# Kernel tuning notes

Hardware: AMD Instinct MI355X
Metric: run time of the kernel (lower is better)

The kernel has to match this reference:

```python
import jax, jax.numpy as jnp
import numpy as np

B, Q, KV, D, H = 2, 2048, 2048, 1024, 16
HD = D // H  # head dim = 64


def setup_inputs() -> dict:
    key = jax.random.key(0)
    ks = jax.random.split(key, 16)
    s = 1.0 / np.sqrt(D)
    return {
        "q": jax.random.normal(ks[0], (B, Q, D), jnp.float32),
        "k": jax.random.normal(ks[1], (B, KV, D), jnp.float32),
        "v": jax.random.normal(ks[2], (B, KV, D), jnp.float32),
        "past_k": jax.random.normal(ks[3], (B, KV, D), jnp.float32),
        "past_v": jax.random.normal(ks[4], (B, KV, D), jnp.float32),
        "mask": jax.random.randint(ks[5], (B, Q, KV + KV), 0, 2).astype(bool),
        "Wq": jax.random.uniform(ks[6], (D, D), jnp.float32, -s, s),
        "bq": jax.random.uniform(ks[7], (D,), jnp.float32, -s, s),
        "Wk": jax.random.uniform(ks[8], (D, D), jnp.float32, -s, s),
        "bk": jax.random.uniform(ks[9], (D,), jnp.float32, -s, s),
        "Wv": jax.random.uniform(ks[10], (D, D), jnp.float32, -s, s),
        "bv": jax.random.uniform(ks[11], (D,), jnp.float32, -s, s),
        "Wl": jax.random.uniform(ks[12], (D, D), jnp.float32, -s, s),
        "bl": jax.random.uniform(ks[13], (D,), jnp.float32, -s, s),
    }


def _split_heads(x):
    # (B, S, D) -> (B, H, S, HD)
    b, s, _ = x.shape
    return x.reshape(b, s, H, HD).transpose(0, 2, 1, 3)


def reference(q, k, v, past_k, past_v, mask, Wq, bq, Wk, bk, Wv, bv, Wl, bl):
    qp = q @ Wq.T + bq
    kp = k @ Wk.T + bk
    vp = v @ Wv.T + bv
    k_cat = jnp.concatenate([past_k, kp], axis=-2)  # (B, P+KV, D)
    v_cat = jnp.concatenate([past_v, vp], axis=-2)
    qh = _split_heads(qp)        # (B, H, Q, HD)
    kh = _split_heads(k_cat)     # (B, H, P+KV, HD)
    vh = _split_heads(v_cat)
    scores = jnp.einsum("bhqd,bhkd->bhqk", qh, kh) / np.sqrt(HD)
    scores = scores + mask[:, None].astype(scores.dtype) * (-10000.0)
    attn = jax.nn.softmax(scores, axis=-1)
    out = jnp.einsum("bhqk,bhkd->bhqd", attn, vh)  # (B, H, Q, HD)
    out = out.transpose(0, 2, 1, 3).reshape(q.shape[0], q.shape[1], D)
    x = out @ Wl.T + bl
    return (x, k_cat, v_cat)
```

## Files before the change

kernel.cpp:

```cpp
#include <hip/hip_runtime.h>

#define QLEN 2048
#define KVTOT 4096
#define DMODEL 1024
#define MASKC -10000.0f
#define SENT  -20000.0f

typedef __attribute__((ext_vector_type(8))) short bf16x8;
typedef __attribute__((ext_vector_type(4))) float f32x4;
typedef unsigned short u16;
typedef unsigned int u32;
typedef unsigned long long u64;

__device__ __forceinline__ u16 f2b(float f) {
  union { float f; unsigned u; } v; v.f = f;
  unsigned r = v.u + 0x7FFFu + ((v.u >> 16) & 1u);
  return (u16)(r >> 16);
}

__device__ __forceinline__ u32 cvt_pk_bf16(float lo, float hi) {
  u32 r;
  asm("v_cvt_pk_bf16_f32 %0, %1, %2" : "=v"(r) : "v"(lo), "v"(hi));
  return r;
}

__device__ __forceinline__ void gll16(const u16* g, u16* l) {
  __builtin_amdgcn_global_load_lds(
      (const __attribute__((address_space(1))) u32*)g,
      (__attribute__((address_space(3))) u32*)l, 16, 0, 0);
}

__global__ __launch_bounds__(256) void copy_past(
    const float* __restrict__ pk, const float* __restrict__ pv,
    float* __restrict__ kcat, float* __restrict__ vcat,
    u16* __restrict__ kh) {
  int i = blockIdx.x * 256 + threadIdx.x;
  int b = i >> 19;
  int r = i & 524287;
  size_t src = (size_t)i * 4;
  size_t dst = ((size_t)b * 1048576 + r) * 4;
  float4 kk = *(const float4*)&pk[src];
  float4 vv = *(const float4*)&pv[src];
  *(float4*)&kcat[dst] = kk;
  *(float4*)&vcat[dst] = vv;
  int s = r >> 8;
  int c4 = (r & 255) * 4;
  int h = c4 >> 6, d = c4 & 63;
  uint2 w = make_uint2(cvt_pk_bf16(kk.x, kk.y), cvt_pk_bf16(kk.z, kk.w));
  *(uint2*)&kh[((size_t)(b * 16 + h) * KVTOT + s) * 64 + d] = w;
}

__global__ __launch_bounds__(256) void maskpack(
    const int* __restrict__ mask, u64* __restrict__ bits) {
  int w = blockIdx.x * 4 + (threadIdx.x >> 6);
  int lane = threadIdx.x & 63;
  int mv = mask[(size_t)w * 64 + lane];
  u64 b = __ballot(mv != 0);
  if (lane == 0) bits[w] = b;
}

__global__ __launch_bounds__(256) void w2b(
    const float* __restrict__ w0, const float* __restrict__ w1,
    const float* __restrict__ w2, const float* __restrict__ w3,
    u16* __restrict__ dst) {
  const float* src = blockIdx.y == 0 ? w0 : blockIdx.y == 1 ? w1
                   : blockIdx.y == 2 ? w2 : w3;
  size_t i = ((size_t)blockIdx.x * 256 + threadIdx.x) * 8;
  float4 a = *(const float4*)&src[i];
  float4 b = *(const float4*)&src[i + 4];
  uint4 o = {cvt_pk_bf16(a.x, a.y), cvt_pk_bf16(a.z, a.w),
             cvt_pk_bf16(b.x, b.y), cvt_pk_bf16(b.z, b.w)};
  *(uint4*)&dst[(size_t)blockIdx.y * 1048576 + i] = o;
}

__global__ __launch_bounds__(256) void gemm_qkv(
    const float* __restrict__ qA, const float* __restrict__ kA,
    const float* __restrict__ vA, const u16* __restrict__ Wb,
    const float* __restrict__ bq, const float* __restrict__ bk,
    const float* __restrict__ bv,
    u16* __restrict__ qh, float* __restrict__ kcat, u16* __restrict__ kh,
    float* __restrict__ vcat) {
  const int K = 1024, N = 1024;
  __shared__ u16 As[128][32];
  __shared__ u16 Bs[128][32];
  const int z = blockIdx.z;
  const float* A = (z == 0) ? qA : (z == 1) ? kA : vA;
  const u16* W = Wb + (size_t)z * 1048576;
  const float* bias = (z == 0) ? bq : (z == 1) ? bk : bv;
  const int t = threadIdx.x;
  const int m0 = blockIdx.y * 128, n0 = blockIdx.x * 128;
  const int lane = t & 63, wid = t >> 6;
  const int wr = (wid >> 1) * 64, wc = (wid & 1) * 64;
  const int lr = lane & 15, lg = lane >> 4;
  const int ko = lg * 8;

  f32x4 acc[4][4];
  #pragma unroll
  for (int m = 0; m < 4; ++m)
    #pragma unroll
    for (int n = 0; n < 4; ++n)
      acc[m][n] = (f32x4){0.f, 0.f, 0.f, 0.f};

  for (int k0 = 0; k0 < K; k0 += 32) {
    float4 a0[2], a1[2];
    #pragma unroll
    for (int j = 0; j < 2; ++j) {
      int idx = t + j * 256;
      int r = idx >> 2, c8 = (idx & 3) * 8;
      const float* ap = A + (size_t)(m0 + r) * K + k0 + c8;
      a0[j] = *(const float4*)ap;
      a1[j] = *(const float4*)(ap + 4);
    }
    __syncthreads();
    #pragma unroll
    for (int j = 0; j < 2; ++j) {
      int idx = t + j * 256;
      int r = idx >> 2, c8 = (idx & 3) * 8;
      gll16(W + (size_t)(n0 + r) * K + k0 + c8,
            &Bs[0][0] + (size_t)(j * 256 + (t & ~63)) * 8);
      uint4 o = {cvt_pk_bf16(a0[j].x, a0[j].y), cvt_pk_bf16(a0[j].z, a0[j].w),
                 cvt_pk_bf16(a1[j].x, a1[j].y), cvt_pk_bf16(a1[j].z, a1[j].w)};
      *(uint4*)&As[r][c8] = o;
    }
    __syncthreads();
    bf16x8 av[4], bv4[4];
    #pragma unroll
    for (int m = 0; m < 4; ++m)
      av[m] = *(const bf16x8*)&As[wr + m * 16 + lr][ko];
    #pragma unroll
    for (int n = 0; n < 4; ++n)
      bv4[n] = *(const bf16x8*)&Bs[wc + n * 16 + lr][ko];
    #pragma unroll
    for (int m = 0; m < 4; ++m)
      #pragma unroll
      for (int n = 0; n < 4; ++n)
        acc[m][n] = __builtin_amdgcn_mfma_f32_16x16x32_bf16(av[m], bv4[n], acc[m][n], 0, 0, 0);
  }

  const int rq = lg * 4;
  #pragma unroll
  for (int m = 0; m < 4; ++m) {
    #pragma unroll
    for (int r = 0; r < 4; ++r) {
      int row = m0 + wr + m * 16 + rq + r;
      int bb = row >> 11, s = row & 2047;
      #pragma unroll
      for (int n = 0; n < 4; ++n) {
        int col = n0 + wc + n * 16 + lr;
        float val = acc[m][n][r] + bias[col];
        int hh = col >> 6, d = col & 63;
        if (z == 0) {
          qh[((size_t)(bb * 16 + hh) * QLEN + s) * 64 + d] = f2b(val * 0.125f);
        } else if (z == 1) {
          kcat[(size_t)(bb * 4096 + 2048 + s) * 1024 + col] = val;
          kh[((size_t)(bb * 16 + hh) * KVTOT + 2048 + s) * 64 + d] = f2b(val);
        } else {
          vcat[(size_t)(bb * 4096 + 2048 + s) * 1024 + col] = val;
        }
      }
    }
  }
}

__global__ __launch_bounds__(256) void gemm_out(
    const u16* __restrict__ A, const u16* __restrict__ W,
    const float* __restrict__ bias, float* __restrict__ C) {
  const int K = 1024, N = 1024;
  __shared__ u16 As[128][32];
  __shared__ u16 Bs[128][32];
  const int t = threadIdx.x;
  const int m0 = blockIdx.y * 128, n0 = blockIdx.x * 128;
  const int lane = t & 63, wid = t >> 6;
  const int wr = (wid >> 1) * 64, wc = (wid & 1) * 64;
  const int lr = lane & 15, lg = lane >> 4;
  const int ko = lg * 8;

  f32x4 acc[4][4];
  #pragma unroll
  for (int m = 0; m < 4; ++m)
    #pragma unroll
    for (int n = 0; n < 4; ++n)
      acc[m][n] = (f32x4){0.f, 0.f, 0.f, 0.f};

  for (int k0 = 0; k0 < K; k0 += 32) {
    __syncthreads();
    #pragma unroll
    for (int j = 0; j < 2; ++j) {
      int idx = t + j * 256;
      int r = idx >> 2, c8 = (idx & 3) * 8;
      size_t ldsoff = (size_t)(j * 256 + (t & ~63)) * 8;
      gll16(A + (size_t)(m0 + r) * K + k0 + c8, &As[0][0] + ldsoff);
      gll16(W + (size_t)(n0 + r) * K + k0 + c8, &Bs[0][0] + ldsoff);
    }
    __syncthreads();
    bf16x8 av[4], bv4[4];
    #pragma unroll
    for (int m = 0; m < 4; ++m)
      av[m] = *(const bf16x8*)&As[wr + m * 16 + lr][ko];
    #pragma unroll
    for (int n = 0; n < 4; ++n)
      bv4[n] = *(const bf16x8*)&Bs[wc + n * 16 + lr][ko];
    #pragma unroll
    for (int m = 0; m < 4; ++m)
      #pragma unroll
      for (int n = 0; n < 4; ++n)
        acc[m][n] = __builtin_amdgcn_mfma_f32_16x16x32_bf16(av[m], bv4[n], acc[m][n], 0, 0, 0);
  }

  const int rq = lg * 4;
  #pragma unroll
  for (int m = 0; m < 4; ++m) {
    #pragma unroll
    for (int r = 0; r < 4; ++r) {
      int row = m0 + wr + m * 16 + rq + r;
      float* cp = C + (size_t)row * N;
      #pragma unroll
      for (int n = 0; n < 4; ++n) {
        int col = n0 + wc + n * 16 + lr;
        cp[col] = acc[m][n][r] + bias[col];
      }
    }
  }
}

__global__ __launch_bounds__(256) void repack_vt(
    const float* __restrict__ src, u16* __restrict__ dst) {
  __shared__ u16 T[64][72];
  const int t = threadIdx.x;
  const int kv0 = blockIdx.x * 64;
  const int bh = blockIdx.y;
  const int b = bh >> 4, h = bh & 15;
  #pragma unroll
  for (int it = 0; it < 4; ++it) {
    int idx = t + it * 256;
    int r = idx >> 4;
    int c4 = (idx & 15) * 4;
    float4 v = *(const float4*)(src + (size_t)(b * KVTOT + kv0 + r) * DMODEL + h * 64 + c4);
    *(uint2*)&T[r][c4] = make_uint2(cvt_pk_bf16(v.x, v.y), cvt_pk_bf16(v.z, v.w));
  }
  __syncthreads();
  #pragma unroll
  for (int it = 0; it < 2; ++it) {
    int idx = t + it * 256;
    int d = idx & 63;
    int kc8 = (idx >> 6) * 8;
    bf16x8 o;
    #pragma unroll
    for (int j = 0; j < 8; ++j) o[j] = (short)T[kc8 + j][d];
    *(bf16x8*)(dst + (size_t)((b * 16 + h) * 64 + d) * KVTOT + kv0 + kc8) = o;
  }
}

__global__ __launch_bounds__(256) void attn_mfma(
    const u16* __restrict__ qh, const u16* __restrict__ kh,
    const u16* __restrict__ vt, const u64* __restrict__ mbits,
    u16* __restrict__ out) {
  __shared__ u16 Kl[64][72];
  __shared__ u16 Vl[64][72];
  __shared__ u16 Pl[4][16][72];
  const int t = threadIdx.x;
  const int wid = t >> 6, lane = t & 63;
  const int lr = lane & 15, lg = lane >> 4;
  const int fid = blockIdx.x;
  const int virt = (fid & 7) * 128 + (fid >> 3);
  const int bh = virt >> 5, qt = virt & 31;
  const int b = bh >> 4, h = bh & 15;
  const int qw = qt * 64 + wid * 16;

  bf16x8 ones;
  #pragma unroll
  for (int j = 0; j < 8; ++j) ones[j] = (short)0x3F80;

  bf16x8 qf[2];
  {
    const u16* qp = qh + ((size_t)bh * QLEN + qw + lr) * 64 + lg * 8;
    qf[0] = *(const bf16x8*)qp;
    qf[1] = *(const bf16x8*)(qp + 32);
  }

  const size_t khb = (size_t)bh * KVTOT * 64;
  const size_t vtb = (size_t)bh * 64 * KVTOT;
  const u64* mrow = mbits + ((size_t)b * QLEN + qw + lr) * (KVTOT / 64);

  bf16x8 kreg[2], vreg[2];
  #pragma unroll
  for (int j = 0; j < 2; ++j) {
    int idx = t + j * 256;
    int r = idx >> 3, c8 = (idx & 7) * 8;
    kreg[j] = *(const bf16x8*)(kh + khb + (size_t)r * 64 + c8);
    vreg[j] = *(const bf16x8*)(vt + vtb + (size_t)r * KVTOT + c8);
  }

  float mprev = SENT;
  f32x4 oacc[5];
  #pragma unroll
  for (int dt = 0; dt < 5; ++dt) oacc[dt] = (f32x4){0.f, 0.f, 0.f, 0.f};

  for (int it = 0; it < KVTOT / 64; ++it) {
    u64 mb = mrow[it];
    __syncthreads();
    #pragma unroll
    for (int j = 0; j < 2; ++j) {
      int idx = t + j * 256;
      int r = idx >> 3, c8 = (idx & 7) * 8;
      *(bf16x8*)&Kl[r][c8] = kreg[j];
      *(bf16x8*)&Vl[r][c8] = vreg[j];
    }
    __syncthreads();
    if (it + 1 < KVTOT / 64) {
      int t0n = (it + 1) * 64;
      #pragma unroll
      for (int j = 0; j < 2; ++j) {
        int idx = t + j * 256;
        int r = idx >> 3, c8 = (idx & 7) * 8;
        kreg[j] = *(const bf16x8*)(kh + khb + (size_t)(t0n + r) * 64 + c8);
        vreg[j] = *(const bf16x8*)(vt + vtb + (size_t)r * KVTOT + t0n + c8);
      }
    }

    const u64 mq = mb >> (lg * 4);
    const float negm = -mprev, negmm = MASKC - mprev;
    f32x4 sacc[4];
    __builtin_amdgcn_s_setprio(1);
    #pragma unroll
    for (int tile = 0; tile < 4; ++tile) {
      unsigned nib = (unsigned)((mq >> (tile * 16)) & 0xFull);
      #pragma unroll
      for (int r = 0; r < 4; ++r)
        sacc[tile][r] = (nib & (1u << r)) ? negmm : negm;
      bf16x8 kf0 = *(const bf16x8*)&Kl[tile * 16 + lr][lg * 8];
      bf16x8 kf1 = *(const bf16x8*)&Kl[tile * 16 + lr][32 + lg * 8];
      sacc[tile] = __builtin_amdgcn_mfma_f32_16x16x32_bf16(kf0, qf[0], sacc[tile], 0, 0, 0);
      sacc[tile] = __builtin_amdgcn_mfma_f32_16x16x32_bf16(kf1, qf[1], sacc[tile], 0, 0, 0);
    }
    __builtin_amdgcn_s_setprio(0);

    float rmax = fmaxf(fmaxf(fmaxf(sacc[0][0], sacc[0][1]), fmaxf(sacc[0][2], sacc[0][3])),
                       fmaxf(fmaxf(sacc[1][0], sacc[1][1]), fmaxf(sacc[1][2], sacc[1][3])));
    rmax = fmaxf(rmax, fmaxf(fmaxf(fmaxf(sacc[2][0], sacc[2][1]), fmaxf(sacc[2][2], sacc[2][3])),
                             fmaxf(fmaxf(sacc[3][0], sacc[3][1]), fmaxf(sacc[3][2], sacc[3][3]))));
    rmax = fmaxf(rmax, __shfl_xor(rmax, 16));
    rmax = fmaxf(rmax, __shfl_xor(rmax, 32));

    if (__all(rmax <= 8.0f)) {
      #pragma unroll
      for (int tile = 0; tile < 4; ++tile) {
        float p0 = __expf(sacc[tile][0]);
        float p1 = __expf(sacc[tile][1]);
        float p2 = __expf(sacc[tile][2]);
        float p3 = __expf(sacc[tile][3]);
        *(uint2*)&Pl[wid][lr][tile * 16 + lg * 4] =
            make_uint2(cvt_pk_bf16(p0, p1), cvt_pk_bf16(p2, p3));
      }
    } else {
      float shift = fmaxf(rmax, 0.f);
      float corr = __expf(-shift);
      float cr[4];
      #pragma unroll
      for (int r = 0; r < 4; ++r) cr[r] = __shfl(corr, lg * 4 + r);
      #pragma unroll
      for (int dt = 0; dt < 5; ++dt)
        #pragma unroll
        for (int r = 0; r < 4; ++r) oacc[dt][r] *= cr[r];
      mprev += shift;
      #pragma unroll
      for (int tile = 0; tile < 4; ++tile) {
        float p0 = __expf(sacc[tile][0] - shift);
        float p1 = __expf(sacc[tile][1] - shift);
        float p2 = __expf(sacc[tile][2] - shift);
        float p3 = __expf(sacc[tile][3] - shift);
        *(uint2*)&Pl[wid][lr][tile * 16 + lg * 4] =
            make_uint2(cvt_pk_bf16(p0, p1), cvt_pk_bf16(p2, p3));
      }
    }

    bf16x8 pa0 = *(const bf16x8*)&Pl[wid][lr][lg * 8];
    bf16x8 pa1 = *(const bf16x8*)&Pl[wid][lr][32 + lg * 8];
    __builtin_amdgcn_s_setprio(1);
    #pragma unroll
    for (int dt = 0; dt < 4; ++dt) {
      bf16x8 vb0 = *(const bf16x8*)&Vl[dt * 16 + lr][lg * 8];
      bf16x8 vb1 = *(const bf16x8*)&Vl[dt * 16 + lr][32 + lg * 8];
      oacc[dt] = __builtin_amdgcn_mfma_f32_16x16x32_bf16(pa0, vb0, oacc[dt], 0, 0, 0);
      oacc[dt] = __builtin_amdgcn_mfma_f32_16x16x32_bf16(pa1, vb1, oacc[dt], 0, 0, 0);
    }
    oacc[4] = __builtin_amdgcn_mfma_f32_16x16x32_bf16(pa0, ones, oacc[4], 0, 0, 0);
    oacc[4] = __builtin_amdgcn_mfma_f32_16x16x32_bf16(pa1, ones, oacc[4], 0, 0, 0);
    __builtin_amdgcn_s_setprio(0);
  }

  #pragma unroll
  for (int r = 0; r < 4; ++r) {
    float inv = 1.f / oacc[4][r];
    #pragma unroll
    for (int dt = 0; dt < 4; ++dt)
      out[((size_t)b * QLEN + qw + lg * 4 + r) * DMODEL + h * 64 + dt * 16 + lr] =
          f2b(oacc[dt][r] * inv);
  }
}

extern "C" void kernel_launch(void* const* d_in, const int* in_sizes, int n_in,
                              void* d_out, int out_size, void* d_ws, size_t ws_size,
                              hipStream_t stream) {
  const float* q      = (const float*)d_in[0];
  const float* k      = (const float*)d_in[1];
  const float* v      = (const float*)d_in[2];
  const float* past_k = (const float*)d_in[3];
  const float* past_v = (const float*)d_in[4];
  const int*   mask   = (const int*)d_in[5];
  const float* Wq     = (const float*)d_in[6];
  const float* bq     = (const float*)d_in[7];
  const float* Wk     = (const float*)d_in[8];
  const float* bk     = (const float*)d_in[9];
  const float* Wv     = (const float*)d_in[10];
  const float* bv     = (const float*)d_in[11];
  const float* Wl     = (const float*)d_in[12];
  const float* bl     = (const float*)d_in[13];

  float* xout = (float*)d_out;
  float* kcat = xout + 4194304;
  float* vcat = xout + 12582912;

  u16* wsb = (u16*)d_ws;
  u16* attno = wsb;
  u16* qh = wsb + 4194304;
  u16* kh = wsb + 8388608;
  u16* vt = wsb + 16777216;
  u16* Wb = wsb + 25165824;
  u64* mbits = (u64*)(wsb + 29360128);

  copy_past<<<4096, 256, 0, stream>>>(past_k, past_v, kcat, vcat, kh);
  maskpack<<<65536, 256, 0, stream>>>(mask, mbits);
  w2b<<<dim3(512, 4), 256, 0, stream>>>(Wq, Wk, Wv, Wl, Wb);

  gemm_qkv<<<dim3(8, 32, 3), 256, 0, stream>>>(
      q, k, v, Wb, bq, bk, bv, qh, kcat, kh, vcat);

  repack_vt<<<dim3(64, 32), 256, 0, stream>>>(vcat, vt);

  attn_mfma<<<1024, 256, 0, stream>>>(qh, kh, vt, mbits, attno);

  gemm_out<<<dim3(8, 32), 256, 0, stream>>>(attno, Wb + 3145728, bl, xout);
}
```

Baseline: 323.3 us.

## Split KV across waves with register-resident K/V and merge partial softmax

Result: slower. 332.1 us (+2.7%).

```diff
diff --git a/kernel.cpp b/kernel.cpp
--- a/kernel.cpp
+++ b/kernel.cpp
@@ -3,8 +3,8 @@
 #define QLEN 2048
 #define KVTOT 4096
 #define DMODEL 1024
-#define MASKC -10000.0f
-#define SENT  -20000.0f
+#define MASKC2 -14427.0f
+#define SENT2  -28854.0f
 
 typedef __attribute__((ext_vector_type(8))) short bf16x8;
 typedef __attribute__((ext_vector_type(4))) float f32x4;
@@ -21,6 +21,18 @@
 __device__ __forceinline__ u32 cvt_pk_bf16(float lo, float hi) {
   u32 r;
   asm("v_cvt_pk_bf16_f32 %0, %1, %2" : "=v"(r) : "v"(lo), "v"(hi));
+  return r;
+}
+
+__device__ __forceinline__ float exp2v(float x) {
+  float r;
+  asm("v_exp_f32 %0, %1" : "=v"(r) : "v"(x));
+  return r;
+}
+
+__device__ __forceinline__ float max3f(float a, float b, float c) {
+  float r;
+  asm("v_max3_f32 %0, %1, %2, %3" : "=v"(r) : "v"(a), "v"(b), "v"(c));
   return r;
 }
 
@@ -150,7 +162,7 @@
         float val = acc[m][n][r] + bias[col];
         int hh = col >> 6, d = col & 63;
         if (z == 0) {
-          qh[((size_t)(bb * 16 + hh) * QLEN + s) * 64 + d] = f2b(val * 0.125f);
+          qh[((size_t)(bb * 16 + hh) * QLEN + s) * 64 + d] = f2b(val * 0.18033688f);
         } else if (z == 1) {
           kcat[(size_t)(bb * 4096 + 2048 + s) * 1024 + col] = val;
           kh[((size_t)(bb * 16 + hh) * KVTOT + 2048 + s) * 64 + d] = f2b(val);
@@ -251,12 +263,13 @@
   }
 }
 
-__global__ __launch_bounds__(256) void attn_mfma(
+__global__ __launch_bounds__(256, 2) void attn_mfma(
     const u16* __restrict__ qh, const u16* __restrict__ kh,
     const u16* __restrict__ vt, const u64* __restrict__ mbits,
     u16* __restrict__ out) {
-  __shared__ u16 Kl[64][72];
-  __shared__ u16 Vl[64][72];
+  __shared__ float mO[4][64][68];
+  __shared__ float mM[4][64];
+  __shared__ float mL[4][64];
   __shared__ u16 Pl[4][16][72];
   const int t = threadIdx.x;
   const int wid = t >> 6, lane = t & 63;
@@ -265,138 +278,182 @@
   const int virt = (fid & 7) * 128 + (fid >> 3);
   const int bh = virt >> 5, qt = virt & 31;
   const int b = bh >> 4, h = bh & 15;
-  const int qw = qt * 64 + wid * 16;
+  const int q0 = qt * 64;
 
   bf16x8 ones;
   #pragma unroll
   for (int j = 0; j < 8; ++j) ones[j] = (short)0x3F80;
 
-  bf16x8 qf[2];
-  {
-    const u16* qp = qh + ((size_t)bh * QLEN + qw + lr) * 64 + lg * 8;
-    qf[0] = *(const bf16x8*)qp;
-    qf[1] = *(const bf16x8*)(qp + 32);
-  }
-
-  const size_t khb = (size_t)bh * KVTOT * 64;
-  const size_t vtb = (size_t)bh * 64 * KVTOT;
-  const u64* mrow = mbits + ((size_t)b * QLEN + qw + lr) * (KVTOT / 64);
-
-  bf16x8 kreg[2], vreg[2];
-  #pragma unroll
-  for (int j = 0; j < 2; ++j) {
-    int idx = t + j * 256;
-    int r = idx >> 3, c8 = (idx & 7) * 8;
-    kreg[j] = *(const bf16x8*)(kh + khb + (size_t)r * 64 + c8);
-    vreg[j] = *(const bf16x8*)(vt + vtb + (size_t)r * KVTOT + c8);
-  }
-
-  float mprev = SENT;
-  f32x4 oacc[5];
-  #pragma unroll
-  for (int dt = 0; dt < 5; ++dt) oacc[dt] = (f32x4){0.f, 0.f, 0.f, 0.f};
-
-  for (int it = 0; it < KVTOT / 64; ++it) {
-    u64 mb = mrow[it];
-    __syncthreads();
-    #pragma unroll
-    for (int j = 0; j < 2; ++j) {
-      int idx = t + j * 256;
-      int r = idx >> 3, c8 = (idx & 7) * 8;
-      *(bf16x8*)&Kl[r][c8] = kreg[j];
-      *(bf16x8*)&Vl[r][c8] = vreg[j];
-    }
-    __syncthreads();
-    if (it + 1 < KVTOT / 64) {
-      int t0n = (it + 1) * 64;
-      #pragma unroll
-      for (int j = 0; j < 2; ++j) {
-        int idx = t + j * 256;
-        int r = idx >> 3, c8 = (idx & 7) * 8;
-        kreg[j] = *(const bf16x8*)(kh + khb + (size_t)(t0n + r) * 64 + c8);
-        vreg[j] = *(const bf16x8*)(vt + vtb + (size_t)r * KVTOT + t0n + c8);
-      }
-    }
-
-    const u64 mq = mb >> (lg * 4);
-    const float negm = -mprev, negmm = MASKC - mprev;
-    f32x4 sacc[4];
-    __builtin_amdgcn_s_setprio(1);
-    #pragma unroll
-    for (int tile = 0; tile < 4; ++tile) {
-      unsigned nib = (unsigned)((mq >> (tile * 16)) & 0xFull);
-      #pragma unroll
-      for (int r = 0; r < 4; ++r)
-        sacc[tile][r] = (nib & (1u << r)) ? negmm : negm;
-      bf16x8 kf0 = *(const bf16x8*)&Kl[tile * 16 + lr][lg * 8];
-      bf16x8 kf1 = *(const bf16x8*)&Kl[tile * 16 + lr][32 + lg * 8];
-      sacc[tile] = __builtin_amdgcn_mfma_f32_16x16x32_bf16(kf0, qf[0], sacc[tile], 0, 0, 0);
-      sacc[tile] = __builtin_amdgcn_mfma_f32_16x16x32_bf16(kf1, qf[1], sacc[tile], 0, 0, 0);
-    }
-    __builtin_amdgcn_s_setprio(0);
-
-    float rmax = fmaxf(fmaxf(fmaxf(sacc[0][0], sacc[0][1]), fmaxf(sacc[0][2], sacc[0][3])),
-                       fmaxf(fmaxf(sacc[1][0], sacc[1][1]), fmaxf(sacc[1][2], sacc[1][3])));
-    rmax = fmaxf(rmax, fmaxf(fmaxf(fmaxf(sacc[2][0], sacc[2][1]), fmaxf(sacc[2][2], sacc[2][3])),
-                             fmaxf(fmaxf(sacc[3][0], sacc[3][1]), fmaxf(sacc[3][2], sacc[3][3]))));
-    rmax = fmaxf(rmax, __shfl_xor(rmax, 16));
-    rmax = fmaxf(rmax, __shfl_xor(rmax, 32));
-
-    if (__all(rmax <= 8.0f)) {
+  bf16x8 qf[4][2];
+  #pragma unroll
+  for (int i = 0; i < 4; ++i) {
+    const u16* qp = qh + ((size_t)bh * QLEN + q0 + i * 16 + lr) * 64 + lg * 8;
+    qf[i][0] = *(const bf16x8*)qp;
+    qf[i][1] = *(const bf16x8*)(qp + 32);
+  }
+
+  const u16* kbase = kh + (size_t)bh * KVTOT * 64 + (size_t)wid * 1024 * 64;
+  const u16* vbase = vt + (size_t)bh * 64 * KVTOT + wid * 1024;
+  const u64* mbase = mbits + ((size_t)b * QLEN + q0 + lr) * 64 + wid * 16;
+
+  float mprev[4] = {SENT2, SENT2, SENT2, SENT2};
+  f32x4 oacc[4][4];
+  f32x4 oaccL[4];
+  #pragma unroll
+  for (int i = 0; i < 4; ++i) {
+    oaccL[i] = (f32x4){0.f, 0.f, 0.f, 0.f};
+    #pragma unroll
+    for (int dt = 0; dt < 4; ++dt) oacc[i][dt] = (f32x4){0.f, 0.f, 0.f, 0.f};
+  }
+
+  bf16x8 kf[4][2];
+  #pragma unroll
+  for (int tile = 0; tile < 4; ++tile) {
+    const u16* kp = kbase + (size_t)(tile * 16 + lr) * 64 + lg * 8;
+    kf[tile][0] = *(const bf16x8*)kp;
+    kf[tile][1] = *(const bf16x8*)(kp + 32);
+  }
+
+  for (int it = 0; it < 16; ++it) {
+    bf16x8 vf[4][2];
+    const u16* vp = vbase + it * 64;
+    #pragma unroll
+    for (int dt = 0; dt < 4; ++dt) {
+      const u16* vq = vp + (size_t)(dt * 16 + lr) * KVTOT + lg * 8;
+      vf[dt][0] = *(const bf16x8*)vq;
+      vf[dt][1] = *(const bf16x8*)(vq + 32);
+    }
+
+    #pragma unroll
+    for (int i = 0; i < 4; ++i) {
+      u64 mb = mbase[(size_t)i * 1024 + it];
+      u64 mq = mb >> (lg * 4);
+      const float negm = -mprev[i], negmm = MASKC2 - mprev[i];
+      f32x4 sacc[4];
       #pragma unroll
       for (int tile = 0; tile < 4; ++tile) {
-        float p0 = __expf(sacc[tile][0]);
-        float p1 = __expf(sacc[tile][1]);
-        float p2 = __expf(sacc[tile][2]);
-        float p3 = __expf(sacc[tile][3]);
+        unsigned nib = (unsigned)((mq >> (tile * 16)) & 0xFull);
+        #pragma unroll
+        for (int r = 0; r < 4; ++r)
+          sacc[tile][r] = (nib & (1u << r)) ? negmm : negm;
+      }
+      __builtin_amdgcn_s_setprio(1);
+      #pragma unroll
+      for (int tile = 0; tile < 4; ++tile) {
+        sacc[tile] = __builtin_amdgcn_mfma_f32_16x16x32_bf16(kf[tile][0], qf[i][0], sacc[tile], 0, 0, 0);
+        sacc[tile] = __builtin_amdgcn_mfma_f32_16x16x32_bf16(kf[tile][1], qf[i][1], sacc[tile], 0, 0, 0);
+      }
+      __builtin_amdgcn_s_setprio(0);
+
+      if (i == 3 && it + 1 < 16) {
+        const u16* kp = kbase + (size_t)(it + 1) * 4096;
+        #pragma unroll
+        for (int tile = 0; tile < 4; ++tile) {
+          const u16* kq = kp + (size_t)(tile * 16 + lr) * 64 + lg * 8;
+          kf[tile][0] = *(const bf16x8*)kq;
+          kf[tile][1] = *(const bf16x8*)(kq + 32);
+        }
+      }
+
+      float t1 = max3f(sacc[0][0], sacc[0][1], sacc[0][2]);
+      float t2 = max3f(sacc[0][3], sacc[1][0], sacc[1][1]);
+      float t3 = max3f(sacc[1][2], sacc[1][3], sacc[2][0]);
+      float t4 = max3f(sacc[2][1], sacc[2][2], sacc[2][3]);
+      float t5 = max3f(sacc[3][0], sacc[3][1], sacc[3][2]);
+      float rmax = fmaxf(sacc[3][3], t1);
+      rmax = max3f(rmax, t2, t3);
+      rmax = max3f(rmax, t4, t5);
+      rmax = fmaxf(rmax, __shfl_xor(rmax, 16));
+      rmax = fmaxf(rmax, __shfl_xor(rmax, 32));
+
+      if (!__all(rmax <= 11.0f)) {
+        float shift = fmaxf(rmax, 0.f);
+        float corr = exp2v(-shift);
+        float cr[4];
+        #pragma unroll
+        for (int r = 0; r < 4; ++r) cr[r] = __shfl(corr, lg * 4 + r);
+        #pragma unroll
+        for (int dt = 0; dt < 4; ++dt)
+          #pragma unroll
+          for (int r = 0; r < 4; ++r) oacc[i][dt][r] *= cr[r];
+        #pragma unroll
+        for (int r = 0; r < 4; ++r) oaccL[i][r] *= cr[r];
+        mprev[i] += shift;
+        #pragma unroll
+        for (int tile = 0; tile < 4; ++tile)
+          #pragma unroll
+          for (int r = 0; r < 4; ++r) sacc[tile][r] -= shift;
+      }
+
+      #pragma unroll
+      for (int tile = 0; tile < 4; ++tile) {
+        float p0 = exp2v(sacc[tile][0]);
+        float p1 = exp2v(sacc[tile][1]);
+        float p2 = exp2v(sacc[tile][2]);
+        float p3 = exp2v(sacc[tile][3]);
         *(uint2*)&Pl[wid][lr][tile * 16 + lg * 4] =
             make_uint2(cvt_pk_bf16(p0, p1), cvt_pk_bf16(p2, p3));
       }
-    } else {
-      float shift = fmaxf(rmax, 0.f);
-      float corr = __expf(-shift);
-      float cr[4];
-      #pragma unroll
-      for (int r = 0; r < 4; ++r) cr[r] = __shfl(corr, lg * 4 + r);
-      #pragma unroll
-      for (int dt = 0; dt < 5; ++dt)
-        #pragma unroll
-        for (int r = 0; r < 4; ++r) oacc[dt][r] *= cr[r];
-      mprev += shift;
-      #pragma unroll
-      for (int tile = 0; tile < 4; ++tile) {
-        float p0 = __expf(sacc[tile][0] - shift);
-        float p1 = __expf(sacc[tile][1] - shift);
-        float p2 = __expf(sacc[tile][2] - shift);
-        float p3 = __expf(sacc[tile][3] - shift);
-        *(uint2*)&Pl[wid][lr][tile * 16 + lg * 4] =
-            make_uint2(cvt_pk_bf16(p0, p1), cvt_pk_bf16(p2, p3));
-      }
-    }
-
-    bf16x8 pa0 = *(const bf16x8*)&Pl[wid][lr][lg * 8];
-    bf16x8 pa1 = *(const bf16x8*)&Pl[wid][lr][32 + lg * 8];
-    __builtin_amdgcn_s_setprio(1);
-    #pragma unroll
-    for (int dt = 0; dt < 4; ++dt) {
-      bf16x8 vb0 = *(const bf16x8*)&Vl[dt * 16 + lr][lg * 8];
-      bf16x8 vb1 = *(const bf16x8*)&Vl[dt * 16 + lr][32 + lg * 8];
-      oacc[dt] = __builtin_amdgcn_mfma_f32_16x16x32_bf16(pa0, vb0, oacc[dt], 0, 0, 0);
-      oacc[dt] = __builtin_amdgcn_mfma_f32_16x16x32_bf16(pa1, vb1, oacc[dt], 0, 0, 0);
-    }
-    oacc[4] = __builtin_amdgcn_mfma_f32_16x16x32_bf16(pa0, ones, oacc[4], 0, 0, 0);
-    oacc[4] = __builtin_amdgcn_mfma_f32_16x16x32_bf16(pa1, ones, oacc[4], 0, 0, 0);
-    __builtin_amdgcn_s_setprio(0);
-  }
-
-  #pragma unroll
-  for (int r = 0; r < 4; ++r) {
-    float inv = 1.f / oacc[4][r];
+      bf16x8 pa0 = *(const bf16x8*)&Pl[wid][lr][lg * 8];
+      bf16x8 pa1 = *(const bf16x8*)&Pl[wid][lr][32 + lg * 8];
+
+      __builtin_amdgcn_s_setprio(1);
+      #pragma unroll
+      for (int dt = 0; dt < 4; ++dt) {
+        oacc[i][dt] = __builtin_amdgcn_mfma_f32_16x16x32_bf16(pa0, vf[dt][0], oacc[i][dt], 0, 0, 0);
+        oacc[i][dt] = __builtin_amdgcn_mfma_f32_16x16x32_bf16(pa1, vf[dt][1], oacc[i][dt], 0, 0, 0);
+      }
+      oaccL[i] = __builtin_amdgcn_mfma_f32_16x16x32_bf16(pa0, ones, oaccL[i], 0, 0, 0);
+      oaccL[i] = __builtin_amdgcn_mfma_f32_16x16x32_bf16(pa1, ones, oaccL[i], 0, 0, 0);
+      __builtin_amdgcn_s_setprio(0);
+    }
+  }
+
+  #pragma unroll
+  for (int i = 0; i < 4; ++i)
     #pragma unroll
     for (int dt = 0; dt < 4; ++dt)
-      out[((size_t)b * QLEN + qw + lg * 4 + r) * DMODEL + h * 64 + dt * 16 + lr] =
-          f2b(oacc[dt][r] * inv);
-  }
+      #pragma unroll
+      for (int r = 0; r < 4; ++r)
+        mO[wid][i * 16 + lg * 4 + r][dt * 16 + lr] = oacc[i][dt][r];
+  if (lr == 0) {
+    #pragma unroll
+    for (int i = 0; i < 4; ++i)
+      #pragma unroll
+      for (int r = 0; r < 4; ++r)
+        mL[wid][i * 16 + lg * 4 + r] = oaccL[i][r];
+  }
+  if (lg == 0) {
+    #pragma unroll
+    for (int i = 0; i < 4; ++i) mM[wid][i * 16 + lr] = mprev[i];
+  }
+  __syncthreads();
+
+  const int q = wid * 16 + lr;
+  float m0 = mM[0][q], m1 = mM[1][q], m2 = mM[2][q], m3 = mM[3][q];
+  float mm = fmaxf(max3f(m0, m1, m2), m3);
+  float w0 = exp2v(m0 - mm), w1 = exp2v(m1 - mm);
+  float w2 = exp2v(m2 - mm), w3 = exp2v(m3 - mm);
+  float l = mL[0][q] * w0 + mL[1][q] * w1 + mL[2][q] * w2 + mL[3][q] * w3;
+  float inv = 1.f / l;
+  float o[16];
+  #pragma unroll
+  for (int c = 0; c < 4; ++c) {
+    f32x4 a0 = *(const f32x4*)&mO[0][q][lg * 16 + c * 4];
+    f32x4 a1 = *(const f32x4*)&mO[1][q][lg * 16 + c * 4];
+    f32x4 a2 = *(const f32x4*)&mO[2][q][lg * 16 + c * 4];
+    f32x4 a3 = *(const f32x4*)&mO[3][q][lg * 16 + c * 4];
+    #pragma unroll
+    for (int j = 0; j < 4; ++j)
+      o[c * 4 + j] = (a0[j] * w0 + a1[j] * w1 + a2[j] * w2 + a3[j] * w3) * inv;
+  }
+  u16* op = out + ((size_t)b * QLEN + q0 + q) * DMODEL + h * 64 + lg * 16;
+  uint4 wA = {cvt_pk_bf16(o[0], o[1]), cvt_pk_bf16(o[2], o[3]),
+              cvt_pk_bf16(o[4], o[5]), cvt_pk_bf16(o[6], o[7])};
+  uint4 wB = {cvt_pk_bf16(o[8], o[9]), cvt_pk_bf16(o[10], o[11]),
+              cvt_pk_bf16(o[12], o[13]), cvt_pk_bf16(o[14], o[15])};
+  *(uint4*)op = wA;
+  *(uint4*)(op + 8) = wB;
 }
 
 extern "C" void kernel_launch(void* const* d_in, const int* in_sizes, int n_in,
```
